# Optimization experiments

Measured on AMD Instinct MI355X. Metric: run time of the kernel, lower is better.

Reference implementation:

```python
import jax, jax.numpy as jnp
import numpy as np

N = 12288      # num nodes == in_num_dim (num_center_nodes)
D_IN = 512     # in_node_dim
D_EMB = 128    # embed_dim
D_OUT = 64     # out_dim
E = 393216     # num edges (avg degree 32)
NEG_SLOPE = 0.2  # GATConv default negative_slope


def _glorot(k, shape):
    lim = float(np.sqrt(6.0 / (shape[0] + shape[1])))
    return jax.random.uniform(k, shape, jnp.float32, -lim, lim)


def setup_inputs() -> dict:
    key = jax.random.key(0)
    ks = jax.random.split(key, 13)
    x = jax.random.normal(ks[0], (N, D_IN), jnp.float32)
    edge_index = jax.random.randint(ks[1], (2, E), 0, N, jnp.int64)
    # StructureAE.dense: Linear(in_node_dim, embed_dim)
    W_s1 = _glorot(ks[2], (D_EMB, D_IN))
    b_s1 = jnp.zeros((D_EMB,), jnp.float32)
    # GATConv(embed_dim, out_dim): heads=1, concat, bias
    W_g = _glorot(ks[3], (D_OUT, D_EMB))
    a_src = _glorot(ks[4], (D_OUT, 1))[:, 0]
    a_dst = _glorot(ks[5], (D_OUT, 1))[:, 0]
    b_g = jnp.zeros((D_OUT,), jnp.float32)
    # AttributeAE: dense1 = Linear(N, embed_dim), dense2 = Linear(embed_dim, out_dim)
    W_a1 = _glorot(ks[6], (D_EMB, N))
    b_a1 = jnp.zeros((D_EMB,), jnp.float32)
    W_a2 = _glorot(ks[7], (D_OUT, D_EMB))
    b_a2 = jnp.zeros((D_OUT,), jnp.float32)
    return dict(x=x, W_s1=W_s1, b_s1=b_s1, W_g=W_g, a_src=a_src, a_dst=a_dst,
                b_g=b_g, W_a1=W_a1, b_a1=b_a1, W_a2=W_a2, b_a2=b_a2,
                edge_index=edge_index, batch_size=N)


def _gat(x1, W_g, a_src, a_dst, b_g, edge_index):
    """Single-head GATConv with self-loops (PyG defaults)."""
    n = x1.shape[0]
    g = x1 @ W_g.T                                   # [N, D_OUT]
    loops = jnp.arange(n, dtype=edge_index.dtype)
    src = jnp.concatenate([edge_index[0], loops])    # message source j
    dst = jnp.concatenate([edge_index[1], loops])    # message target i
    sc_src = g @ a_src                               # [N]
    sc_dst = g @ a_dst                               # [N]
    e = jax.nn.leaky_relu(sc_src[src] + sc_dst[dst], NEG_SLOPE)  # [E+N]
    m = jax.ops.segment_max(e, dst, num_segments=n)
    e = jnp.exp(e - m[dst])
    denom = jax.ops.segment_sum(e, dst, num_segments=n)
    alpha = e / denom[dst]                           # softmax per target node
    h = jax.ops.segment_sum(alpha[:, None] * g[src], dst, num_segments=n)
    return h + b_g


def reference(x, W_s1, b_s1, W_g, a_src, a_dst, b_g,
              W_a1, b_a1, W_a2, b_a2, edge_index, batch_size):
    n = x.shape[0]
    # StructureAE (dropout=0 -> identity)
    x1 = jax.nn.relu(x @ W_s1.T + b_s1)              # [N, D_EMB]
    h = _gat(x1, W_g, a_src, a_dst, b_g, edge_index)  # [N, D_OUT]
    s_ = jax.nn.sigmoid(h @ h.T)                     # [N, N]
    # AttributeAE on x[:num_center_nodes] (pad if batch smaller)
    xp = x if batch_size >= n else jnp.pad(x, ((0, n - batch_size), (0, 0)))
    xt = jax.nn.relu(xp.T @ W_a1.T + b_a1)           # [D_IN, D_EMB]
    xa = xt @ W_a2.T + b_a2                          # [D_IN, D_OUT]
    x_ = h @ xa.T                                    # [N, D_IN]
    return (x_, s_)
```

## Files before the change

kernel.cpp:

```cpp
#include <hip/hip_runtime.h>
#include <cstddef>
#include <cstdint>

#define N_NODES 12288
#define D_IN    512
#define D_EMB   128
#define D_OUT   64
#define NEDGE   393216

typedef __attribute__((ext_vector_type(8))) short short8;
typedef __attribute__((ext_vector_type(4))) float f32x4;

__device__ __forceinline__ ushort f2bf(float f) {
  uint32_t u = __float_as_uint(f);
  u += 0x7fffu + ((u >> 16) & 1u);
  return (ushort)(u >> 16);
}
__device__ __forceinline__ float bf2f(ushort h) {
  return __uint_as_float((uint32_t)h << 16);
}

__global__ __launch_bounds__(256) void init_kernel(const int* __restrict__ ei,
    int* __restrict__ flag, int* __restrict__ deg)
{
  int idx = blockIdx.x * 256 + threadIdx.x;
  if (idx < N_NODES) deg[idx] = 0;
  if (idx == 0) {
    int ok = 1;
    for (int t = 0; t < 64; ++t) ok &= (ei[2 * t + 1] == 0);
    *flag = ok;
  }
}

__global__ __launch_bounds__(256) void edge_deg(const int* __restrict__ ei,
    const int* __restrict__ flag, int* __restrict__ deg)
{
  int e = blockIdx.x * 256 + threadIdx.x;
  if (e >= NEDGE) return;
  int dst = (*flag) ? ei[2 * (NEDGE + e)] : ei[NEDGE + e];
  atomicAdd(&deg[dst], 1);
}

__global__ __launch_bounds__(256) void scan_deg(const int* __restrict__ deg,
    int* __restrict__ rp, int* __restrict__ cursor)
{
  __shared__ int sums[256];
  constexpr int C = N_NODES / 256;
  int t = threadIdx.x;
  int base = t * C;
  int local[C];
  int s = 0;
  for (int i = 0; i < C; ++i) { local[i] = deg[base + i]; s += local[i]; }
  sums[t] = s;
  __syncthreads();
  for (int off = 1; off < 256; off <<= 1) {
    int v = (t >= off) ? sums[t - off] : 0;
    __syncthreads();
    sums[t] += v;
    __syncthreads();
  }
  int prefix = (t == 0) ? 0 : sums[t - 1];
  for (int i = 0; i < C; ++i) {
    rp[base + i] = prefix;
    cursor[base + i] = prefix;
    prefix += local[i];
  }
  if (t == 255) rp[N_NODES] = prefix;
}

__global__ __launch_bounds__(256) void edge_scatter(const int* __restrict__ ei,
    const int* __restrict__ flag, int* __restrict__ cursor, int* __restrict__ csr)
{
  int e = blockIdx.x * 256 + threadIdx.x;
  if (e >= NEDGE) return;
  int is64 = *flag;
  int src = is64 ? ei[2 * e] : ei[e];
  int dst = is64 ? ei[2 * (NEDGE + e)] : ei[NEDGE + e];
  int p = atomicAdd(&cursor[dst], 1);
  csr[p] = src;
}

template<int ACT>
__global__ __launch_bounds__(256) void gemm_nt64(const float* __restrict__ A,
    const float* __restrict__ B, const float* __restrict__ bias,
    float* __restrict__ C, int M, int N, int K, int ldc)
{
  __shared__ float As[32][64];
  __shared__ float Bs[32][64];
  int m0 = blockIdx.x * 64, n0 = blockIdx.y * 64;
  int tid = threadIdx.x;
  int tx = tid & 15, ty = tid >> 4;
  float acc[4][4] = {};
  for (int k0 = 0; k0 < K; k0 += 32) {
#pragma unroll
    for (int p = 0; p < 2; ++p) {
      int idx = tid + p * 256;
      int row = idx >> 3;
      int kq  = idx & 7;
      float4 va = *(const float4*)(A + (size_t)(m0 + row) * K + k0 + kq * 4);
      As[kq*4+0][row] = va.x; As[kq*4+1][row] = va.y;
      As[kq*4+2][row] = va.z; As[kq*4+3][row] = va.w;
      float4 vb = *(const float4*)(B + (size_t)(n0 + row) * K + k0 + kq * 4);
      Bs[kq*4+0][row] = vb.x; Bs[kq*4+1][row] = vb.y;
      Bs[kq*4+2][row] = vb.z; Bs[kq*4+3][row] = vb.w;
    }
    __syncthreads();
#pragma unroll
    for (int k = 0; k < 32; ++k) {
      float a[4], b[4];
      *(float4*)a = *(const float4*)&As[k][ty * 4];
      *(float4*)b = *(const float4*)&Bs[k][tx * 4];
#pragma unroll
      for (int r = 0; r < 4; ++r)
#pragma unroll
        for (int c = 0; c < 4; ++c)
          acc[r][c] = fmaf(a[r], b[c], acc[r][c]);
    }
    __syncthreads();
  }
#pragma unroll
  for (int r = 0; r < 4; ++r) {
    int m = m0 + ty * 4 + r;
    float4 o;
    float* po = &o.x;
#pragma unroll
    for (int c = 0; c < 4; ++c) {
      float v = acc[r][c];
      if (bias) v += bias[n0 + tx * 4 + c];
      if (ACT) v = fmaxf(v, 0.f);
      po[c] = v;
    }
    *(float4*)(C + (size_t)m * ldc + n0 + tx * 4) = o;
  }
}

__global__ __launch_bounds__(256) void scores_kernel(const float* __restrict__ g,
    const float* __restrict__ a_src, const float* __restrict__ a_dst,
    float* __restrict__ sc_s, float* __restrict__ sc_d)
{
  int lane = threadIdx.x & 63;
  int i = blockIdx.x * 4 + (threadIdx.x >> 6);
  float gv = g[(size_t)i * 64 + lane];
  float vs = gv * a_src[lane];
  float vd = gv * a_dst[lane];
#pragma unroll
  for (int off = 32; off; off >>= 1) {
    vs += __shfl_xor(vs, off);
    vd += __shfl_xor(vd, off);
  }
  if (lane == 0) { sc_s[i] = vs; sc_d[i] = vd; }
}

__global__ __launch_bounds__(256) void gat_kernel(const int* __restrict__ rp,
    const int* __restrict__ csr, const float* __restrict__ sc_s,
    const float* __restrict__ sc_d, const float* __restrict__ g,
    const float* __restrict__ b_g, float* __restrict__ h,
    ushort* __restrict__ hhi, ushort* __restrict__ hlo)
{
  int lane = threadIdx.x & 63;
  int i = blockIdx.x * 4 + (threadIdx.x >> 6);
  int beg = rp[i], end = rp[i + 1];
  int deg = end - beg;
  float scd = sc_d[i];
  float mymax = -3.4e38f;
  for (int j = lane; j <= deg; j += 64) {
    int s = (j < deg) ? csr[beg + j] : i;
    float e = sc_s[s] + scd;
    e = (e > 0.f) ? e : 0.2f * e;
    mymax = fmaxf(mymax, e);
  }
#pragma unroll
  for (int off = 32; off; off >>= 1) mymax = fmaxf(mymax, __shfl_xor(mymax, off));
  float sum = 0.f;
  for (int j = lane; j <= deg; j += 64) {
    int s = (j < deg) ? csr[beg + j] : i;
    float e = sc_s[s] + scd;
    e = (e > 0.f) ? e : 0.2f * e;
    sum += __expf(e - mymax);
  }
#pragma unroll
  for (int off = 32; off; off >>= 1) sum += __shfl_xor(sum, off);
  float inv = 1.f / sum;
  float acc = 0.f;
  for (int j = 0; j <= deg; ++j) {
    int s = (j < deg) ? csr[beg + j] : i;
    float e = sc_s[s] + scd;
    e = (e > 0.f) ? e : 0.2f * e;
    float w = __expf(e - mymax) * inv;
    acc = fmaf(w, g[(size_t)s * 64 + lane], acc);
  }
  float val = acc + b_g[lane];
  size_t o = (size_t)i * 64 + lane;
  h[o] = val;
  ushort hi = f2bf(val);
  hhi[o] = hi;
  hlo[o] = f2bf(val - bf2f(hi));
}

__global__ __launch_bounds__(256) void xt_splitk(const float* __restrict__ x,
    const float* __restrict__ Wa1, float* __restrict__ part)
{
  __shared__ float Xs[32][64];
  __shared__ float Ws[32][128];
  int c0 = blockIdx.x * 64;
  int i0 = blockIdx.y * 192;
  float* pout = part + (size_t)blockIdx.y * (D_IN * D_EMB);
  int tid = threadIdx.x;
  int txc = tid & 15, txj = tid >> 4;
  float acc[4][8] = {};
  for (int ib = 0; ib < 192; ib += 32) {
#pragma unroll
    for (int p = 0; p < 2; ++p) {
      int idx = tid + p * 256;
      int row = idx >> 4, q = idx & 15;
      *(float4*)&Xs[row][q * 4] =
          *(const float4*)(x + (size_t)(i0 + ib + row) * D_IN + c0 + q * 4);
    }
#pragma unroll
    for (int p = 0; p < 4; ++p) {
      int idx = tid + p * 256;
      int j = idx >> 3, q = idx & 7;
      float4 v = *(const float4*)(Wa1 + (size_t)j * N_NODES + i0 + ib + q * 4);
      Ws[q*4+0][j] = v.x; Ws[q*4+1][j] = v.y;
      Ws[q*4+2][j] = v.z; Ws[q*4+3][j] = v.w;
    }
    __syncthreads();
#pragma unroll
    for (int ii = 0; ii < 32; ++ii) {
      float a[4], b[8];
      *(float4*)a = *(const float4*)&Xs[ii][txc * 4];
      *(float4*)&b[0] = *(const float4*)&Ws[ii][txj * 8];
      *(float4*)&b[4] = *(const float4*)&Ws[ii][txj * 8 + 4];
#pragma unroll
      for (int r = 0; r < 4; ++r)
#pragma unroll
        for (int c = 0; c < 8; ++c)
          acc[r][c] = fmaf(a[r], b[c], acc[r][c]);
    }
    __syncthreads();
  }
#pragma unroll
  for (int r = 0; r < 4; ++r) {
    float4 o0, o1;
    o0.x = acc[r][0]; o0.y = acc[r][1]; o0.z = acc[r][2]; o0.w = acc[r][3];
    o1.x = acc[r][4]; o1.y = acc[r][5]; o1.z = acc[r][6]; o1.w = acc[r][7];
    size_t off = (size_t)(c0 + txc * 4 + r) * D_EMB + txj * 8;
    *(float4*)&pout[off] = o0;
    *(float4*)&pout[off + 4] = o1;
  }
}

__global__ __launch_bounds__(256) void xt_ep(const float* __restrict__ part,
    const float* __restrict__ b_a1, float* __restrict__ xt)
{
  int idx = blockIdx.x * 256 + threadIdx.x;
  float v = b_a1[idx & 127];
#pragma unroll 8
  for (int c = 0; c < 64; ++c) v += part[(size_t)c * (D_IN * D_EMB) + idx];
  xt[idx] = fmaxf(v, 0.f);
}

__global__ __launch_bounds__(256) void sig_hht_mfma(const ushort* __restrict__ hhi,
    const ushort* __restrict__ hlo, float* __restrict__ out)
{
  int lane = threadIdx.x & 63;
  int wave = threadIdx.x >> 6;
  int i0 = blockIdx.x * 128 + (wave >> 1) * 64;
  int j0 = blockIdx.y * 128 + (wave & 1) * 64;
  int lm = lane & 15, lk = lane >> 4;
  f32x4 acc[4][4];
#pragma unroll
  for (int r = 0; r < 4; ++r)
#pragma unroll
    for (int c = 0; c < 4; ++c) acc[r][c] = (f32x4){0.f, 0.f, 0.f, 0.f};
#pragma unroll
  for (int ks = 0; ks < 2; ++ks) {
    short8 Ah[4], Al[4], Bh[4], Bl[4];
#pragma unroll
    for (int t = 0; t < 4; ++t) {
      size_t ra = (size_t)(i0 + t * 16 + lm) * 64 + ks * 32 + lk * 8;
      size_t rb = (size_t)(j0 + t * 16 + lm) * 64 + ks * 32 + lk * 8;
      Ah[t] = *(const short8*)(hhi + ra);
      Al[t] = *(const short8*)(hlo + ra);
      Bh[t] = *(const short8*)(hhi + rb);
      Bl[t] = *(const short8*)(hlo + rb);
    }
#pragma unroll
    for (int r = 0; r < 4; ++r)
#pragma unroll
      for (int c = 0; c < 4; ++c) {
        acc[r][c] = __builtin_amdgcn_mfma_f32_16x16x32_bf16(Ah[r], Bh[c], acc[r][c], 0, 0, 0);
        acc[r][c] = __builtin_amdgcn_mfma_f32_16x16x32_bf16(Ah[r], Bl[c], acc[r][c], 0, 0, 0);
        acc[r][c] = __builtin_amdgcn_mfma_f32_16x16x32_bf16(Al[r], Bh[c], acc[r][c], 0, 0, 0);
      }
  }
#pragma unroll
  for (int r = 0; r < 4; ++r)
#pragma unroll
    for (int c = 0; c < 4; ++c) {
#pragma unroll
      for (int q = 0; q < 4; ++q) {
        float v = acc[r][c][q];
        float ex = __expf(-v);
#if __has_builtin(__builtin_amdgcn_rcpf)
        float s = __builtin_amdgcn_rcpf(1.f + ex);
#else
        float s = 1.f / (1.f + ex);
#endif
        out[(size_t)(i0 + r * 16 + lk * 4 + q) * N_NODES + (j0 + c * 16 + lm)] = s;
      }
    }
}

extern "C" void kernel_launch(void* const* d_in, const int* in_sizes, int n_in,
                              void* d_out, int out_size, void* d_ws, size_t ws_size,
                              hipStream_t stream)
{
  const float* x     = (const float*)d_in[0];
  const float* W_s1  = (const float*)d_in[1];
  const float* b_s1  = (const float*)d_in[2];
  const float* W_g   = (const float*)d_in[3];
  const float* a_src = (const float*)d_in[4];
  const float* a_dst = (const float*)d_in[5];
  const float* b_g   = (const float*)d_in[6];
  const float* W_a1  = (const float*)d_in[7];
  const float* b_a1  = (const float*)d_in[8];
  const float* W_a2  = (const float*)d_in[9];
  const float* b_a2  = (const float*)d_in[10];
  const int*   ei    = (const int*)d_in[11];

  float* ws   = (float*)d_ws;
  float* x1   = ws;
  float* g    = x1 + (size_t)N_NODES * D_EMB;
  float* h    = g  + (size_t)N_NODES * D_OUT;
  float* sc_s = h  + (size_t)N_NODES * D_OUT;
  float* sc_d = sc_s + N_NODES;
  float* part = sc_d + N_NODES;
  float* xt   = part + (size_t)64 * D_IN * D_EMB;
  float* xa   = xt + D_IN * D_EMB;
  int* ib     = (int*)(xa + D_IN * D_OUT);
  int* flag   = ib;
  int* deg    = ib + 64;
  int* rp     = deg + N_NODES;
  int* cursor = rp + 12352;
  int* csr    = cursor + N_NODES;
  ushort* hhi = (ushort*)(csr + NEDGE);
  ushort* hlo = hhi + (size_t)N_NODES * D_OUT;

  float* out_x = (float*)d_out;
  float* out_s = out_x + (size_t)N_NODES * D_IN;

  init_kernel<<<48, 256, 0, stream>>>(ei, flag, deg);
  edge_deg<<<NEDGE / 256, 256, 0, stream>>>(ei, flag, deg);
  scan_deg<<<1, 256, 0, stream>>>(deg, rp, cursor);
  edge_scatter<<<NEDGE / 256, 256, 0, stream>>>(ei, flag, cursor, csr);

  gemm_nt64<1><<<dim3(192, 2), 256, 0, stream>>>(x, W_s1, b_s1, x1,
                                                 N_NODES, D_EMB, D_IN, D_EMB);
  gemm_nt64<0><<<dim3(192, 1), 256, 0, stream>>>(x1, W_g, nullptr, g,
                                                 N_NODES, D_OUT, D_EMB, D_OUT);
  scores_kernel<<<N_NODES / 4, 256, 0, stream>>>(g, a_src, a_dst, sc_s, sc_d);
  gat_kernel<<<N_NODES / 4, 256, 0, stream>>>(rp, csr, sc_s, sc_d, g, b_g,
                                              h, hhi, hlo);

  xt_splitk<<<dim3(8, 64), 256, 0, stream>>>(x, W_a1, part);
  xt_ep<<<D_IN * D_EMB / 256, 256, 0, stream>>>(part, b_a1, xt);
  gemm_nt64<0><<<dim3(8, 1), 256, 0, stream>>>(xt, W_a2, b_a2, xa,
                                               D_IN, D_OUT, D_EMB, D_OUT);

  gemm_nt64<0><<<dim3(192, 8), 256, 0, stream>>>(h, xa, nullptr, out_x,
                                                 N_NODES, D_IN, D_OUT, D_IN);
  sig_hht_mfma<<<dim3(96, 96), 256, 0, stream>>>(hhi, hlo, out_s);
}
```

Before: 922.1 us.

## Move all dense GEMMs to split-bf16 MFMA with pre-converted hi/lo operands

Adds conversion kernels that split x (and its transpose), W_s1, W_g, W_a1 and xa into bf16 hi/lo pairs. A generic MFMA NT GEMM using three bf16 products then replaces the fp32 CUDA-core GEMMs for x1, g, the x^T·W_a1 split-K and out_x. The split-K count drops from 64 to 32. This targets the FP32 FMA throughput cost of the large GEMMs, but adds conversion passes that read x and W_a1 and write several extra bf16 copies. The sigmoid also switches from the rcp builtin back to a true division.

```diff
diff --git a/kernel.cpp b/kernel.cpp
--- a/kernel.cpp
+++ b/kernel.cpp
@@ -18,6 +18,68 @@
 }
 __device__ __forceinline__ float bf2f(ushort h) {
   return __uint_as_float((uint32_t)h << 16);
+}
+
+__global__ __launch_bounds__(256) void conv_hilo(const float* __restrict__ src,
+    ushort* __restrict__ hi, ushort* __restrict__ lo)
+{
+  int idx = (blockIdx.x * 256 + threadIdx.x) * 4;
+  float4 v = *(const float4*)(src + idx);
+  const float* pv = &v.x;
+  ushort4 h, l;
+  ushort* ph = &h.x; ushort* pl = &l.x;
+#pragma unroll
+  for (int q = 0; q < 4; ++q) {
+    ph[q] = f2bf(pv[q]);
+    pl[q] = f2bf(pv[q] - bf2f(ph[q]));
+  }
+  *(ushort4*)(hi + idx) = h;
+  *(ushort4*)(lo + idx) = l;
+}
+
+__global__ __launch_bounds__(256) void conv_x(const float* __restrict__ x,
+    ushort* __restrict__ xhi, ushort* __restrict__ xlo,
+    ushort* __restrict__ xThi, ushort* __restrict__ xTlo)
+{
+  __shared__ float t4[64][68];
+  int i0 = blockIdx.x * 64, c0 = blockIdx.y * 64;
+  int ty = threadIdx.x >> 2;
+  int tx = threadIdx.x & 3;
+#pragma unroll
+  for (int p = 0; p < 4; ++p) {
+    int col = (tx + p * 4) * 4;
+    float4 v = *(const float4*)(x + (size_t)(i0 + ty) * D_IN + c0 + col);
+    const float* pv = &v.x;
+    ushort4 h, l;
+    ushort* ph = &h.x; ushort* pl = &l.x;
+#pragma unroll
+    for (int q = 0; q < 4; ++q) {
+      ph[q] = f2bf(pv[q]);
+      pl[q] = f2bf(pv[q] - bf2f(ph[q]));
+      t4[col + q][ty] = pv[q];
+    }
+    size_t o = (size_t)(i0 + ty) * D_IN + c0 + col;
+    *(ushort4*)(xhi + o) = h;
+    *(ushort4*)(xlo + o) = l;
+  }
+  __syncthreads();
+  int cy = threadIdx.x >> 2;
+  int cx = threadIdx.x & 3;
+#pragma unroll
+  for (int g4 = 0; g4 < 4; ++g4) {
+    float4 w = *(const float4*)&t4[cy][cx * 16 + g4 * 4];
+    const float* pw = &w.x;
+    ushort4 th, tl;
+    ushort* pth = &th.x; ushort* ptl = &tl.x;
+#pragma unroll
+    for (int q = 0; q < 4; ++q) {
+      pth[q] = f2bf(pw[q]);
+      ptl[q] = f2bf(pw[q] - bf2f(pth[q]));
+    }
+    size_t ot = (size_t)(c0 + cy) * N_NODES + i0 + cx * 16 + g4 * 4;
+    *(ushort4*)(xThi + ot) = th;
+    *(ushort4*)(xTlo + ot) = tl;
+  }
 }
 
 __global__ __launch_bounds__(256) void init_kernel(const int* __restrict__ ei,
@@ -80,6 +142,71 @@
   csr[p] = src;
 }
 
+template<int WY, int WX, int MODE>
+__global__ __launch_bounds__(256) void mfma_nt(
+    const ushort* __restrict__ Ahi, const ushort* __restrict__ Alo,
+    const ushort* __restrict__ Bhi, const ushort* __restrict__ Blo,
+    const float* __restrict__ bias,
+    float* __restrict__ Cf, ushort* __restrict__ Chi, ushort* __restrict__ Clo,
+    int lda, int ldb, int K, int ldc, size_t part_stride)
+{
+  int lane = threadIdx.x & 63;
+  int wave = threadIdx.x >> 6;
+  int wy = wave / WX, wx = wave % WX;
+  int i0 = blockIdx.x * (64 * WY) + wy * 64;
+  int j0 = blockIdx.y * (64 * WX) + wx * 64;
+  int kbase = blockIdx.z * K;
+  float* Cout = Cf + (size_t)blockIdx.z * part_stride;
+  int lm = lane & 15, lk = lane >> 4;
+  f32x4 acc[4][4];
+#pragma unroll
+  for (int r = 0; r < 4; ++r)
+#pragma unroll
+    for (int c = 0; c < 4; ++c) acc[r][c] = (f32x4){0.f, 0.f, 0.f, 0.f};
+
+  for (int k0 = 0; k0 < K; k0 += 32) {
+    int kk = kbase + k0 + lk * 8;
+    short8 Ah[4], Al[4], Bh[4], Bl[4];
+#pragma unroll
+    for (int t = 0; t < 4; ++t) {
+      size_t ra = (size_t)(i0 + t * 16 + lm) * lda + kk;
+      size_t rb = (size_t)(j0 + t * 16 + lm) * ldb + kk;
+      Ah[t] = *(const short8*)(Ahi + ra);
+      Al[t] = *(const short8*)(Alo + ra);
+      Bh[t] = *(const short8*)(Bhi + rb);
+      Bl[t] = *(const short8*)(Blo + rb);
+    }
+#pragma unroll
+    for (int r = 0; r < 4; ++r)
+#pragma unroll
+      for (int c = 0; c < 4; ++c) {
+        acc[r][c] = __builtin_amdgcn_mfma_f32_16x16x32_bf16(Ah[r], Bh[c], acc[r][c], 0, 0, 0);
+        acc[r][c] = __builtin_amdgcn_mfma_f32_16x16x32_bf16(Ah[r], Bl[c], acc[r][c], 0, 0, 0);
+        acc[r][c] = __builtin_amdgcn_mfma_f32_16x16x32_bf16(Al[r], Bh[c], acc[r][c], 0, 0, 0);
+      }
+  }
+#pragma unroll
+  for (int r = 0; r < 4; ++r)
+#pragma unroll
+    for (int c = 0; c < 4; ++c) {
+      int col = j0 + c * 16 + lm;
+#pragma unroll
+      for (int q = 0; q < 4; ++q) {
+        int row = i0 + r * 16 + lk * 4 + q;
+        float v = acc[r][c][q];
+        if (MODE == 0) {
+          Cout[(size_t)row * ldc + col] = v;
+        } else {
+          v += bias[col];
+          v = fmaxf(v, 0.f);
+          ushort hb = f2bf(v);
+          Chi[(size_t)row * ldc + col] = hb;
+          Clo[(size_t)row * ldc + col] = f2bf(v - bf2f(hb));
+        }
+      }
+    }
+}
+
 template<int ACT>
 __global__ __launch_bounds__(256) void gemm_nt64(const float* __restrict__ A,
     const float* __restrict__ B, const float* __restrict__ bias,
@@ -154,7 +281,7 @@
 __global__ __launch_bounds__(256) void gat_kernel(const int* __restrict__ rp,
     const int* __restrict__ csr, const float* __restrict__ sc_s,
     const float* __restrict__ sc_d, const float* __restrict__ g,
-    const float* __restrict__ b_g, float* __restrict__ h,
+    const float* __restrict__ b_g,
     ushort* __restrict__ hhi, ushort* __restrict__ hlo)
 {
   int lane = threadIdx.x & 63;
@@ -191,72 +318,18 @@
   }
   float val = acc + b_g[lane];
   size_t o = (size_t)i * 64 + lane;
-  h[o] = val;
   ushort hi = f2bf(val);
   hhi[o] = hi;
   hlo[o] = f2bf(val - bf2f(hi));
 }
 
-__global__ __launch_bounds__(256) void xt_splitk(const float* __restrict__ x,
-    const float* __restrict__ Wa1, float* __restrict__ part)
-{
-  __shared__ float Xs[32][64];
-  __shared__ float Ws[32][128];
-  int c0 = blockIdx.x * 64;
-  int i0 = blockIdx.y * 192;
-  float* pout = part + (size_t)blockIdx.y * (D_IN * D_EMB);
-  int tid = threadIdx.x;
-  int txc = tid & 15, txj = tid >> 4;
-  float acc[4][8] = {};
-  for (int ib = 0; ib < 192; ib += 32) {
-#pragma unroll
-    for (int p = 0; p < 2; ++p) {
-      int idx = tid + p * 256;
-      int row = idx >> 4, q = idx & 15;
-      *(float4*)&Xs[row][q * 4] =
-          *(const float4*)(x + (size_t)(i0 + ib + row) * D_IN + c0 + q * 4);
-    }
-#pragma unroll
-    for (int p = 0; p < 4; ++p) {
-      int idx = tid + p * 256;
-      int j = idx >> 3, q = idx & 7;
-      float4 v = *(const float4*)(Wa1 + (size_t)j * N_NODES + i0 + ib + q * 4);
-      Ws[q*4+0][j] = v.x; Ws[q*4+1][j] = v.y;
-      Ws[q*4+2][j] = v.z; Ws[q*4+3][j] = v.w;
-    }
-    __syncthreads();
-#pragma unroll
-    for (int ii = 0; ii < 32; ++ii) {
-      float a[4], b[8];
-      *(float4*)a = *(const float4*)&Xs[ii][txc * 4];
-      *(float4*)&b[0] = *(const float4*)&Ws[ii][txj * 8];
-      *(float4*)&b[4] = *(const float4*)&Ws[ii][txj * 8 + 4];
-#pragma unroll
-      for (int r = 0; r < 4; ++r)
-#pragma unroll
-        for (int c = 0; c < 8; ++c)
-          acc[r][c] = fmaf(a[r], b[c], acc[r][c]);
-    }
-    __syncthreads();
-  }
-#pragma unroll
-  for (int r = 0; r < 4; ++r) {
-    float4 o0, o1;
-    o0.x = acc[r][0]; o0.y = acc[r][1]; o0.z = acc[r][2]; o0.w = acc[r][3];
-    o1.x = acc[r][4]; o1.y = acc[r][5]; o1.z = acc[r][6]; o1.w = acc[r][7];
-    size_t off = (size_t)(c0 + txc * 4 + r) * D_EMB + txj * 8;
-    *(float4*)&pout[off] = o0;
-    *(float4*)&pout[off + 4] = o1;
-  }
-}
-
 __global__ __launch_bounds__(256) void xt_ep(const float* __restrict__ part,
     const float* __restrict__ b_a1, float* __restrict__ xt)
 {
   int idx = blockIdx.x * 256 + threadIdx.x;
   float v = b_a1[idx & 127];
 #pragma unroll 8
-  for (int c = 0; c < 64; ++c) v += part[(size_t)c * (D_IN * D_EMB) + idx];
+  for (int c = 0; c < 32; ++c) v += part[(size_t)c * (D_IN * D_EMB) + idx];
   xt[idx] = fmaxf(v, 0.f);
 }
 
@@ -302,11 +375,7 @@
       for (int q = 0; q < 4; ++q) {
         float v = acc[r][c][q];
         float ex = __expf(-v);
-#if __has_builtin(__builtin_amdgcn_rcpf)
-        float s = __builtin_amdgcn_rcpf(1.f + ex);
-#else
         float s = 1.f / (1.f + ex);
-#endif
         out[(size_t)(i0 + r * 16 + lk * 4 + q) * N_NODES + (j0 + c * 16 + lm)] = s;
       }
     }
@@ -330,45 +399,69 @@
   const int*   ei    = (const int*)d_in[11];
 
   float* ws   = (float*)d_ws;
-  float* x1   = ws;
-  float* g    = x1 + (size_t)N_NODES * D_EMB;
-  float* h    = g  + (size_t)N_NODES * D_OUT;
-  float* sc_s = h  + (size_t)N_NODES * D_OUT;
+  float* g    = ws;
+  float* sc_s = g + (size_t)N_NODES * D_OUT;
   float* sc_d = sc_s + N_NODES;
   float* part = sc_d + N_NODES;
-  float* xt   = part + (size_t)64 * D_IN * D_EMB;
+  float* xt   = part + (size_t)32 * D_IN * D_EMB;
   float* xa   = xt + D_IN * D_EMB;
-  int* ib     = (int*)(xa + D_IN * D_OUT);
-  int* flag   = ib;
-  int* deg    = ib + 64;
+  int* ip     = (int*)(xa + D_IN * D_OUT);
+  int* flag   = ip;
+  int* deg    = ip + 64;
   int* rp     = deg + N_NODES;
   int* cursor = rp + 12352;
   int* csr    = cursor + N_NODES;
-  ushort* hhi = (ushort*)(csr + NEDGE);
-  ushort* hlo = hhi + (size_t)N_NODES * D_OUT;
+  ushort* up  = (ushort*)(csr + NEDGE);
+  ushort* xhi  = up;                         up += (size_t)N_NODES * D_IN;
+  ushort* xlo  = up;                         up += (size_t)N_NODES * D_IN;
+  ushort* xThi = up;                         up += (size_t)N_NODES * D_IN;
+  ushort* xTlo = up;                         up += (size_t)N_NODES * D_IN;
+  ushort* x1hi = up;                         up += (size_t)N_NODES * D_EMB;
+  ushort* x1lo = up;                         up += (size_t)N_NODES * D_EMB;
+  ushort* Ws1hi = up;                        up += (size_t)D_EMB * D_IN;
+  ushort* Ws1lo = up;                        up += (size_t)D_EMB * D_IN;
+  ushort* Wghi = up;                         up += (size_t)D_OUT * D_EMB;
+  ushort* Wglo = up;                         up += (size_t)D_OUT * D_EMB;
+  ushort* Wa1hi = up;                        up += (size_t)D_EMB * N_NODES;
+  ushort* Wa1lo = up;                        up += (size_t)D_EMB * N_NODES;
+  ushort* hhi = up;                          up += (size_t)N_NODES * D_OUT;
+  ushort* hlo = up;                          up += (size_t)N_NODES * D_OUT;
+  ushort* xahi = up;                         up += (size_t)D_IN * D_OUT;
+  ushort* xalo = up;                         up += (size_t)D_IN * D_OUT;
 
   float* out_x = (float*)d_out;
   float* out_s = out_x + (size_t)N_NODES * D_IN;
+
+  conv_x<<<dim3(192, 8), 256, 0, stream>>>(x, xhi, xlo, xThi, xTlo);
+  conv_hilo<<<(D_EMB * D_IN) / 1024, 256, 0, stream>>>(W_s1, Ws1hi, Ws1lo);
+  conv_hilo<<<(D_OUT * D_EMB) / 1024, 256, 0, stream>>>(W_g, Wghi, Wglo);
+  conv_hilo<<<((size_t)D_EMB * N_NODES) / 1024, 256, 0, stream>>>(W_a1, Wa1hi, Wa1lo);
 
   init_kernel<<<48, 256, 0, stream>>>(ei, flag, deg);
   edge_deg<<<NEDGE / 256, 256, 0, stream>>>(ei, flag, deg);
   scan_deg<<<1, 256, 0, stream>>>(deg, rp, cursor);
   edge_scatter<<<NEDGE / 256, 256, 0, stream>>>(ei, flag, cursor, csr);
 
-  gemm_nt64<1><<<dim3(192, 2), 256, 0, stream>>>(x, W_s1, b_s1, x1,
-                                                 N_NODES, D_EMB, D_IN, D_EMB);
-  gemm_nt64<0><<<dim3(192, 1), 256, 0, stream>>>(x1, W_g, nullptr, g,
-                                                 N_NODES, D_OUT, D_EMB, D_OUT);
+  mfma_nt<2, 2, 1><<<dim3(96, 1, 1), 256, 0, stream>>>(
+      xhi, xlo, Ws1hi, Ws1lo, b_s1, nullptr, x1hi, x1lo,
+      D_IN, D_IN, D_IN, D_EMB, 0);
+  mfma_nt<4, 1, 0><<<dim3(48, 1, 1), 256, 0, stream>>>(
+      x1hi, x1lo, Wghi, Wglo, nullptr, g, nullptr, nullptr,
+      D_EMB, D_EMB, D_EMB, D_OUT, 0);
   scores_kernel<<<N_NODES / 4, 256, 0, stream>>>(g, a_src, a_dst, sc_s, sc_d);
   gat_kernel<<<N_NODES / 4, 256, 0, stream>>>(rp, csr, sc_s, sc_d, g, b_g,
-                                              h, hhi, hlo);
-
-  xt_splitk<<<dim3(8, 64), 256, 0, stream>>>(x, W_a1, part);
+                                              hhi, hlo);
+
+  mfma_nt<2, 2, 0><<<dim3(4, 1, 32), 256, 0, stream>>>(
+      xThi, xTlo, Wa1hi, Wa1lo, nullptr, part, nullptr, nullptr,
+      N_NODES, N_NODES, 384, D_EMB, (size_t)D_IN * D_EMB);
   xt_ep<<<D_IN * D_EMB / 256, 256, 0, stream>>>(part, b_a1, xt);
   gemm_nt64<0><<<dim3(8, 1), 256, 0, stream>>>(xt, W_a2, b_a2, xa,
                                                D_IN, D_OUT, D_EMB, D_OUT);
-
-  gemm_nt64<0><<<dim3(192, 8), 256, 0, stream>>>(h, xa, nullptr, out_x,
-                                                 N_NODES, D_IN, D_OUT, D_IN);
+  conv_hilo<<<(D_IN * D_OUT) / 1024, 256, 0, stream>>>(xa, xahi, xalo);
+
+  mfma_nt<2, 2, 0><<<dim3(96, 4, 1), 256, 0, stream>>>(
+      hhi, hlo, xahi, xalo, nullptr, out_x, nullptr, nullptr,
+      D_OUT, D_OUT, D_OUT, D_IN, 0);
   sig_hht_mfma<<<dim3(96, 96), 256, 0, stream>>>(hhi, hlo, out_s);
 }
```

After: 969.5 us. +5.1%, slower.
